# Kernel optimization log

Hardware: AMD Instinct MI355X
Metric: run time of the kernel (lower is better)

Reference implementation:

```python
import jax, jax.numpy as jnp
import numpy as np

# --- static config (lmax = mmax = 2, m-prime coefficient layout) ---
L = 2
NCOEF = (L + 1) ** 2            # 9 coeffs; m-prime order: m=0 -> l=0,1,2 | m=1 -> (-,+) x l=1,2 | m=2 -> (-,+) x l=2
GATE_IDX = jnp.array([0, 1, 0, 1, 0, 1, 1, 1])  # (l-1) of each non-scalar coeff in m-prime order
N_NODES = 10000
N_EDGES = 50000
C_SPH = 128
C_HID = 128
C_EDGE = 128
EXTRA_M0 = L * C_HID            # gate scalars emitted by conv1's m=0 branch


def _silu(x):
    return x * jax.nn.sigmoid(x)


def _layernorm(x, g, b, eps=1e-5):
    mu = jnp.mean(x, axis=-1, keepdims=True)
    var = jnp.var(x, axis=-1, keepdims=True)
    return (x - mu) * jax.lax.rsqrt(var + eps) * g + b


def _radial(x_edge, w1, b1, g, beta, w2, b2):
    # RadialFunction: Linear -> LayerNorm -> SiLU -> Linear, emits per-edge channel weights [E, 6*c_in]
    h = _silu(_layernorm(x_edge @ w1 + b1, g, beta))
    return h @ w2 + b2


def _so2_conv(feat, rad, w0, b0, w1, w2, c_in, c_out, extra):
    # feat: [E, 9, c_in] in m-prime order. Block-diagonal SO2 conv with per-edge radial modulation.
    E = feat.shape[0]
    # m = 0 block (3 real coeffs) -> dense linear, optionally emits extra gating scalars
    x0 = feat[:, 0:3].reshape(E, 3 * c_in) * rad[:, : 3 * c_in]
    y0 = x0 @ w0 + b0                                   # [E, 3*c_out + extra]
    out0 = y0[:, : 3 * c_out].reshape(E, 3, c_out)
    x_extra = y0[:, 3 * c_out:]
    # m = 1 block: coeffs 3:7 -> [E, 2(sign), 2(l)*c_in], complex-structured matmul
    x1 = feat[:, 3:7].reshape(E, 2, 2 * c_in) * rad[:, 3 * c_in: 5 * c_in][:, None, :]
    y1 = x1 @ w1                                        # [E, 2, 4*c_out]
    h = 2 * c_out
    r, i = y1[..., :h], y1[..., h:]
    out1 = jnp.stack([r[:, 0] - i[:, 1], r[:, 1] + i[:, 0]], axis=1).reshape(E, 4, c_out)
    # m = 2 block: coeffs 7:9 -> [E, 2(sign), 1(l)*c_in]
    x2 = feat[:, 7:9].reshape(E, 2, c_in) * rad[:, 5 * c_in: 6 * c_in][:, None, :]
    y2 = x2 @ w2                                        # [E, 2, 2*c_out]
    r, i = y2[..., :c_out], y2[..., c_out:]
    out2 = jnp.stack([r[:, 0] - i[:, 1], r[:, 1] + i[:, 0]], axis=1).reshape(E, 2, c_out)
    return jnp.concatenate([out0, out1, out2], axis=1), x_extra


def _gate(gating, feat):
    # GateActivation (m_prime=True): SiLU on l=0 scalar, SiLU(gates) broadcast per-degree on l>0 coeffs
    E = feat.shape[0]
    g = _silu(gating).reshape(E, L, C_HID)[:, GATE_IDX]  # [E, 8, C_HID]
    return jnp.concatenate([_silu(feat[:, :1]), feat[:, 1:] * g], axis=1)


def setup_inputs() -> dict:
    key = jax.random.key(0)
    ks = jax.random.split(key, 16)

    def nrm(k, shape, scale=1.0):
        return jax.random.normal(k, shape, dtype=jnp.float32) * scale

    C, H, CE = C_SPH, C_HID, C_EDGE
    return {
        "x": nrm(ks[0], (N_NODES, NCOEF, C)),
        "x_edge": nrm(ks[1], (N_EDGES, CE)),
        "edge_distance": jax.random.uniform(ks[2], (N_EDGES,), dtype=jnp.float32),
        "edge_index": jax.random.randint(ks[3], (2, N_EDGES), 0, N_NODES),
        "wigner": nrm(ks[4], (N_EDGES, NCOEF, NCOEF), 0.3),
        "wigner_inv": nrm(ks[5], (N_EDGES, NCOEF, NCOEF), 0.3),
        # radial MLP 1 (edge embed -> 6*C_SPH per-edge weights)
        "rad1_w1": nrm(ks[6], (CE, CE), CE ** -0.5),
        "rad1_b1": jnp.zeros((CE,), jnp.float32),
        "rad1_g": jnp.ones((CE,), jnp.float32),
        "rad1_beta": jnp.zeros((CE,), jnp.float32),
        "rad1_w2": nrm(ks[7], (CE, 6 * C), CE ** -0.5),
        "rad1_b2": jnp.zeros((6 * C,), jnp.float32),
        # SO2 conv 1 (sphere -> hidden, + gate scalars)
        "c1_w0": nrm(ks[8], (3 * C, 3 * H + EXTRA_M0), (3 * C) ** -0.5),
        "c1_b0": jnp.zeros((3 * H + EXTRA_M0,), jnp.float32),
        "c1_w1": nrm(ks[9], (2 * C, 4 * H), (2 * C) ** -0.5),
        "c1_w2": nrm(ks[10], (C, 2 * H), C ** -0.5),
        # radial MLP 2 (edge embed -> 6*C_HID per-edge weights)
        "rad2_w1": nrm(ks[11], (CE, CE), CE ** -0.5),
        "rad2_b1": jnp.zeros((CE,), jnp.float32),
        "rad2_g": jnp.ones((CE,), jnp.float32),
        "rad2_beta": jnp.zeros((CE,), jnp.float32),
        "rad2_w2": nrm(ks[12], (CE, 6 * H), CE ** -0.5),
        "rad2_b2": jnp.zeros((6 * H,), jnp.float32),
        # SO2 conv 2 (hidden -> sphere)
        "c2_w0": nrm(ks[13], (3 * H, 3 * C), (3 * H) ** -0.5),
        "c2_b0": jnp.zeros((3 * C,), jnp.float32),
        "c2_w1": nrm(ks[14], (2 * H, 4 * C), (2 * H) ** -0.5),
        "c2_w2": nrm(ks[15], (H, 2 * C), H ** -0.5),
    }


def reference(x, x_edge, edge_distance, edge_index, wigner, wigner_inv,
              rad1_w1, rad1_b1, rad1_g, rad1_beta, rad1_w2, rad1_b2,
              c1_w0, c1_b0, c1_w1, c1_w2,
              rad2_w1, rad2_b1, rad2_g, rad2_beta, rad2_w2, rad2_b2,
              c2_w0, c2_b0, c2_w1, c2_w2):
    src, dst = edge_index[0], edge_index[1]
    # gather source node features + per-edge Wigner rotation into m-prime layout: [E, 9, C_SPH]
    msg = jnp.einsum('erf,efc->erc', wigner, x[src])
    rad1 = _radial(x_edge, rad1_w1, rad1_b1, rad1_g, rad1_beta, rad1_w2, rad1_b2)
    msg, gating = _so2_conv(msg, rad1, c1_w0, c1_b0, c1_w1, c1_w2, C_SPH, C_HID, EXTRA_M0)
    msg = _gate(gating, msg)
    rad2 = _radial(x_edge, rad2_w1, rad2_b1, rad2_g, rad2_beta, rad2_w2, rad2_b2)
    msg, _ = _so2_conv(msg, rad2, c2_w0, c2_b0, c2_w1, c2_w2, C_HID, C_SPH, 0)
    # rotate back to the global frame and scatter-sum onto destination nodes
    msg = jnp.einsum('efr,erc->efc', wigner_inv, msg)
    return jax.ops.segment_sum(msg, dst, num_segments=x.shape[0])
```

## Files before the change

kernel.cpp:

```cpp
#include <hip/hip_runtime.h>
#include <hip/hip_bf16.h>

#define EDGES 50000
#define NODES 10000

typedef __hip_bfloat16 bf16;
typedef __attribute__((ext_vector_type(8))) short bf16x8v;
typedef __attribute__((ext_vector_type(4))) float f32x4;

__device__ __forceinline__ float bf2f(bf16 v){ return __bfloat162float(v); }
__device__ __forceinline__ bf16  f2bf(float v){ return __float2bfloat16(v); }
__device__ __forceinline__ unsigned short f2bfu(float f){
  bf16 h = __float2bfloat16(f);
  union{ bf16 h; unsigned short s; } u; u.h = h; return u.s;
}
__device__ __forceinline__ float silu_f(float v){ return v * (1.0f/(1.0f+__expf(-v))); }

__device__ __forceinline__ unsigned mul1(unsigned a, unsigned b){
  union{unsigned u; float f;} a0,a1,b0,b1;
  a0.u = (a & 0xffffu) << 16; a1.u = a & 0xffff0000u;
  b0.u = (b & 0xffffu) << 16; b1.u = b & 0xffff0000u;
  float p0 = a0.f*b0.f, p1 = a1.f*b1.f;
  return (unsigned)f2bfu(p0) | ((unsigned)f2bfu(p1) << 16);
}
__device__ __forceinline__ uint4 mulp(uint4 a, uint4 b){
  uint4 r; r.x=mul1(a.x,b.x); r.y=mul1(a.y,b.y); r.z=mul1(a.z,b.z); r.w=mul1(a.w,b.w); return r;
}

__global__ __launch_bounds__(256)
void k_wT(const float* __restrict__ w, bf16* __restrict__ wt, int K, int N){
  __shared__ float tile[32][33];
  const int kb = blockIdx.x*32, nb = blockIdx.y*32;
  const int tx = threadIdx.x & 31, ty = threadIdx.x >> 5;
#pragma unroll
  for (int i=0;i<32;i+=8) tile[ty+i][tx] = w[(size_t)(kb+ty+i)*N + nb+tx];
  __syncthreads();
#pragma unroll
  for (int i=0;i<32;i+=8) wt[(size_t)(nb+ty+i)*K + kb+tx] = f2bf(tile[tx][ty+i]);
}

__global__ __launch_bounds__(128)
void k_gather_rot(const float* __restrict__ x, const int* __restrict__ eidx,
                  const float* __restrict__ wig, bf16* __restrict__ msg)
{
  const int e = blockIdx.x;
  const int c = threadIdx.x;
  __shared__ float wl[81];
  if (c < 81) wl[c] = wig[e*81 + c];
  const int src = eidx[e];
  const float* xp = x + (size_t)src*1152 + c;
  float xr[9];
#pragma unroll
  for (int f=0; f<9; ++f) xr[f] = xp[f*128];
  __syncthreads();
  bf16* mp = msg + (size_t)e*1152 + c;
#pragma unroll
  for (int fo=0; fo<9; ++fo){
    float a = 0.f;
#pragma unroll
    for (int f=0; f<9; ++f) a = fmaf(wl[fo*9+f], xr[f], a);
    mp[fo*128] = f2bf(a);
  }
}

__global__ __launch_bounds__(256)
void k_radial(const float* __restrict__ x_edge,
              const float* __restrict__ w1, const float* __restrict__ b1,
              const float* __restrict__ gm, const float* __restrict__ bt,
              const float* __restrict__ w2, const float* __restrict__ b2,
              bf16* __restrict__ ro)
{
  __shared__ float xe[16][128];
  __shared__ float h[16][128];
  __shared__ float mu_s[16], rs_s[16];
  const int t = threadIdx.x;
  const int e0 = blockIdx.x * 16;
  for (int i=0;i<8;++i){
    int lin = t + 256*i;
    int e = lin >> 7, j2 = lin & 127;
    xe[e][j2] = x_edge[(size_t)(e0+e)*128 + j2];
  }
  __syncthreads();
  const int j = t & 127, g = t >> 7;
  {
    float acc[8] = {0,0,0,0,0,0,0,0};
    for (int k=0;k<128;k+=4){
      float wv0 = w1[(k+0)*128+j];
      float wv1 = w1[(k+1)*128+j];
      float wv2 = w1[(k+2)*128+j];
      float wv3 = w1[(k+3)*128+j];
#pragma unroll
      for (int e=0;e<8;++e){
        float4 xv = *(const float4*)&xe[g*8+e][k];
        acc[e] += xv.x*wv0 + xv.y*wv1 + xv.z*wv2 + xv.w*wv3;
      }
    }
    float bv = b1[j];
#pragma unroll
    for (int e=0;e<8;++e) h[g*8+e][j] = acc[e] + bv;
  }
  __syncthreads();
  {
    int e = t >> 4, p = t & 15;
    float s=0.f, ss=0.f;
#pragma unroll
    for (int i=0;i<8;++i){ float v = h[e][p+16*i]; s += v; ss += v*v; }
#pragma unroll
    for (int off=8; off>0; off>>=1){ s += __shfl_xor(s, off, 16); ss += __shfl_xor(ss, off, 16); }
    if (p==0){
      float m = s*(1.f/128.f);
      mu_s[e] = m;
      rs_s[e] = rsqrtf(fmaxf(ss*(1.f/128.f)-m*m, 0.f) + 1e-5f);
    }
  }
  __syncthreads();
  {
    float gv = gm[j], bv = bt[j];
#pragma unroll
    for (int e=0;e<8;++e){
      int ee = g*8+e;
      float v = (h[ee][j]-mu_s[ee])*rs_s[ee]*gv + bv;
      h[ee][j] = silu_f(v);
    }
  }
  __syncthreads();
  if (t < 192){
    int col = t*4;
    float acc[16][4];
#pragma unroll
    for (int e=0;e<16;++e){ acc[e][0]=acc[e][1]=acc[e][2]=acc[e][3]=0.f; }
    for (int k=0;k<128;k+=4){
      float4 wv0 = *(const float4*)&w2[(k+0)*768+col];
      float4 wv1 = *(const float4*)&w2[(k+1)*768+col];
      float4 wv2 = *(const float4*)&w2[(k+2)*768+col];
      float4 wv3 = *(const float4*)&w2[(k+3)*768+col];
#pragma unroll
      for (int e=0;e<16;++e){
        float4 hv = *(const float4*)&h[e][k];
        acc[e][0] += hv.x*wv0.x + hv.y*wv1.x + hv.z*wv2.x + hv.w*wv3.x;
        acc[e][1] += hv.x*wv0.y + hv.y*wv1.y + hv.z*wv2.y + hv.w*wv3.y;
        acc[e][2] += hv.x*wv0.z + hv.y*wv1.z + hv.z*wv2.z + hv.w*wv3.z;
        acc[e][3] += hv.x*wv0.w + hv.y*wv1.w + hv.z*wv2.w + hv.w*wv3.w;
      }
    }
    float4 bv = *(const float4*)&b2[col];
#pragma unroll
    for (int e=0;e<16;++e){
      ushort4 pk;
      pk.x = f2bfu(acc[e][0]+bv.x);
      pk.y = f2bfu(acc[e][1]+bv.y);
      pk.z = f2bfu(acc[e][2]+bv.z);
      pk.w = f2bfu(acc[e][3]+bv.w);
      *reinterpret_cast<ushort4*>(&ro[(size_t)(e0+e)*768 + col]) = pk;
    }
  }
}


template<bool CONV1>
__global__ __launch_bounds__(256, 3)
void k_g0(const bf16* __restrict__ rad, const bf16* __restrict__ msg_in,
          const bf16* __restrict__ w0t, const float* __restrict__ b0,
          bf16* __restrict__ msg, bf16* __restrict__ glb)
{
  __shared__ char ldsA[24576];
  __shared__ bf16 gls[8192];
  const int t = threadIdx.x;
  const int lane = t & 63, wv = t >> 6;
  const int lrow = lane & 15, lhi = lane >> 4;
  const int e0 = blockIdx.x * 32;
  int evalid = EDGES - e0; if (evalid > 32) evalid = 32;
  const uint4 z4 = {0u,0u,0u,0u};
  const f32x4 zf = {0.f,0.f,0.f,0.f};

#pragma unroll
  for (int i=0;i<6;++i){
    int ch = t + 256*i;
    int row = ch / 48, k0 = (ch % 48) * 8;
    int e = e0 + row;
    uint4 mz = z4, rz = z4;
    if (e < EDGES){
      mz = *(const uint4*)(msg_in + (size_t)e*1152 + k0);
      rz = *(const uint4*)(rad    + (size_t)e*768  + k0);
    }
    *(uint4*)(ldsA + ((row*768 + k0*2) ^ ((row&7)<<4))) = mulp(mz, rz);
  }
  __syncthreads();

  constexpr int NT0 = CONV1 ? 10 : 6;
  constexpr int HB  = NT0 / 2;
  const int wcol0 = wv * NT0 * 16;
  f32x4 acc0[NT0][2];
#pragma unroll
  for (int nt=0; nt<NT0; ++nt){ acc0[nt][0]=zf; acc0[nt][1]=zf; }
  for (int ks=0; ks<12; ++ks){
    bf16x8v a0 = *(const bf16x8v*)(ldsA + (((lrow   )*768 + ks*64 + lhi*16) ^ ((lrow&7)<<4)));
    bf16x8v a1 = *(const bf16x8v*)(ldsA + (((16+lrow)*768 + ks*64 + lhi*16) ^ ((lrow&7)<<4)));
#pragma unroll
    for (int h=0; h<2; ++h){
      bf16x8v bb[HB];
#pragma unroll
      for (int j=0;j<HB;++j){
        int coln = wcol0 + (h*HB+j)*16 + lrow;
        bb[j] = *(const bf16x8v*)(w0t + (size_t)coln*384 + ks*32 + lhi*8);
      }
#pragma unroll
      for (int j=0;j<HB;++j){
        int nt = h*HB+j;
        acc0[nt][0] = __builtin_amdgcn_mfma_f32_16x16x32_bf16(a0, bb[j], acc0[nt][0], 0,0,0);
        acc0[nt][1] = __builtin_amdgcn_mfma_f32_16x16x32_bf16(a1, bb[j], acc0[nt][1], 0,0,0);
      }
    }
  }
  if (CONV1){
#pragma unroll
    for (int nt=0; nt<NT0; ++nt){
      int colb = wcol0 + nt*16;
      if (colb >= 384){
        float bc = b0[colb + lrow];
        int cc = colb + lrow - 384;
#pragma unroll
        for (int mt=0; mt<2; ++mt)
#pragma unroll
        for (int r=0; r<4; ++r){
          int el = mt*16 + lhi*4 + r;
          bf16 gv = f2bf(silu_f(acc0[nt][mt][r] + bc));
          gls[el*256 + cc] = gv;
          if (el < evalid) glb[(size_t)(e0+el)*256 + cc] = gv;
        }
      }
    }
    __syncthreads();
  }
#pragma unroll
  for (int nt=0; nt<NT0; ++nt){
    int colb = wcol0 + nt*16;
    if (colb < 384){
      int col = colb + lrow;
      int f = col >> 7, c = col & 127;
      float bc = b0[col];
#pragma unroll
      for (int mt=0; mt<2; ++mt)
#pragma unroll
      for (int r=0; r<4; ++r){
        int el = mt*16 + lhi*4 + r;
        if (el < evalid){
          float v = acc0[nt][mt][r] + bc;
          float o;
          if (CONV1) o = (f==0) ? silu_f(v) : v * bf2f(gls[el*256 + (f==2?128:0) + c]);
          else       o = v;
          msg[(size_t)(e0+el)*1152 + col] = f2bf(o);
        }
      }
    }
  }
}

template<bool CONV1>
__global__ __launch_bounds__(256, 3)
void k_g1(const bf16* __restrict__ rad,
          const bf16* __restrict__ w1t,
          bf16* __restrict__ msg, const bf16* __restrict__ glb)
{
  __shared__ char ldsA[16384];
  const int t = threadIdx.x;
  const int lane = t & 63, wv = t >> 6;
  const int lrow = lane & 15, lhi = lane >> 4;
  const int e0 = blockIdx.x * 16;
  const uint4 z4 = {0u,0u,0u,0u};
  const f32x4 zf = {0.f,0.f,0.f,0.f};

#pragma unroll
  for (int i=0;i<4;++i){
    int ch = t + 256*i;
    int row = ch >> 5, k0 = (ch & 31) * 8;
    int e = e0 + (row >> 1);
    uint4 mz = z4, rz = z4;
    if (e < EDGES){
      mz = *(const uint4*)(msg + (size_t)e*1152 + 384 + (row&1)*256 + k0);
      rz = *(const uint4*)(rad + (size_t)e*768  + 384 + k0);
    }
    *(uint4*)(ldsA + ((row*512 + k0*2) ^ ((row&7)<<4))) = mulp(mz, rz);
  }
  __syncthreads();

  f32x4 acc1[4][2][2];
#pragma unroll
  for (int p=0;p<4;++p){ acc1[p][0][0]=zf; acc1[p][0][1]=zf; acc1[p][1][0]=zf; acc1[p][1][1]=zf; }
  for (int ks=0; ks<8; ++ks){
    bf16x8v aA[2];
#pragma unroll
    for (int m2=0; m2<2; ++m2){
      int row = m2*16 + lrow;
      aA[m2] = *(const bf16x8v*)(ldsA + ((row*512 + ks*64 + lhi*16) ^ ((row&7)<<4)));
    }
    bf16x8v br[4], bi[4];
#pragma unroll
    for (int p=0; p<4; ++p){
      int jj = wv*64 + p*16 + lrow;
      br[p] = *(const bf16x8v*)(w1t + (size_t)jj*256       + ks*32 + lhi*8);
      bi[p] = *(const bf16x8v*)(w1t + (size_t)(jj+256)*256 + ks*32 + lhi*8);
    }
#pragma unroll
    for (int p=0; p<4; ++p)
#pragma unroll
    for (int m2=0;m2<2;++m2){
      acc1[p][m2][0] = __builtin_amdgcn_mfma_f32_16x16x32_bf16(aA[m2], br[p], acc1[p][m2][0], 0,0,0);
      acc1[p][m2][1] = __builtin_amdgcn_mfma_f32_16x16x32_bf16(aA[m2], bi[p], acc1[p][m2][1], 0,0,0);
    }
  }
#pragma unroll
  for (int p=0;p<4;++p)
#pragma unroll
  for (int m2=0;m2<2;++m2)
#pragma unroll
  for (int re=0;re<2;++re){
    int elL = m2*8 + lhi*2 + re;
    int e = e0 + elL;
    if (e < EDGES){
      float r0 = acc1[p][m2][0][2*re+0], r1 = acc1[p][m2][0][2*re+1];
      float i0 = acc1[p][m2][1][2*re+0], i1 = acc1[p][m2][1][2*re+1];
      float o0 = r0 - i1, o1 = r1 + i0;
      int jj = wv*64 + p*16 + lrow;
      if (CONV1){ float g = bf2f(glb[(size_t)e*256 + jj]); o0 *= g; o1 *= g; }
      size_t base = (size_t)e*1152;
      msg[base + 384 + jj] = f2bf(o0);
      msg[base + 640 + jj] = f2bf(o1);
    }
  }
}

template<bool CONV1>
__global__ __launch_bounds__(256, 3)
void k_g2(const bf16* __restrict__ rad,
          const bf16* __restrict__ w2t,
          bf16* __restrict__ msg, const bf16* __restrict__ glb)
{
  __shared__ char ldsA[16384];
  const int t = threadIdx.x;
  const int lane = t & 63, wv = t >> 6;
  const int lrow = lane & 15, lhi = lane >> 4;
  const int e0 = blockIdx.x * 32;
  const uint4 z4 = {0u,0u,0u,0u};
  const f32x4 zf = {0.f,0.f,0.f,0.f};

#pragma unroll
  for (int i=0;i<4;++i){
    int ch = t + 256*i;
    int row = ch >> 4, k0 = (ch & 15) * 8;
    int e = e0 + (row >> 1);
    uint4 mz = z4, rz = z4;
    if (e < EDGES){
      mz = *(const uint4*)(msg + (size_t)e*1152 + 896 + (row&1)*128 + k0);
      rz = *(const uint4*)(rad + (size_t)e*768  + 640 + k0);
    }
    *(uint4*)(ldsA + ((row*256 + k0*2) ^ ((row&7)<<4))) = mulp(mz, rz);
  }
  __syncthreads();

  f32x4 acc2[2][4][2];
#pragma unroll
  for (int p=0;p<2;++p)
#pragma unroll
  for (int mt=0;mt<4;++mt){ acc2[p][mt][0]=zf; acc2[p][mt][1]=zf; }
  for (int ks=0; ks<4; ++ks){
    bf16x8v aA[4];
#pragma unroll
    for (int mt=0;mt<4;++mt){
      int row = mt*16 + lrow;
      aA[mt] = *(const bf16x8v*)(ldsA + ((row*256 + ks*64 + lhi*16) ^ ((row&7)<<4)));
    }
    bf16x8v br2[2], bi2[2];
#pragma unroll
    for (int p=0;p<2;++p){
      int jj = wv*32 + p*16 + lrow;
      br2[p] = *(const bf16x8v*)(w2t + (size_t)jj*128       + ks*32 + lhi*8);
      bi2[p] = *(const bf16x8v*)(w2t + (size_t)(jj+128)*128 + ks*32 + lhi*8);
    }
#pragma unroll
    for (int p=0;p<2;++p)
#pragma unroll
    for (int mt=0;mt<4;++mt){
      acc2[p][mt][0] = __builtin_amdgcn_mfma_f32_16x16x32_bf16(aA[mt], br2[p], acc2[p][mt][0], 0,0,0);
      acc2[p][mt][1] = __builtin_amdgcn_mfma_f32_16x16x32_bf16(aA[mt], bi2[p], acc2[p][mt][1], 0,0,0);
    }
  }
#pragma unroll
  for (int p=0;p<2;++p)
#pragma unroll
  for (int mt=0;mt<4;++mt)
#pragma unroll
  for (int re=0;re<2;++re){
    int el = mt*8 + lhi*2 + re;
    int e = e0 + el;
    if (e < EDGES){
      float r0 = acc2[p][mt][0][2*re+0], r1 = acc2[p][mt][0][2*re+1];
      float i0 = acc2[p][mt][1][2*re+0], i1 = acc2[p][mt][1][2*re+1];
      float o0 = r0 - i1, o1 = r1 + i0;
      int jj = wv*32 + p*16 + lrow;
      if (CONV1){ float g = bf2f(glb[(size_t)e*256 + 128 + jj]); o0 *= g; o1 *= g; }
      size_t base = (size_t)e*1152;
      msg[base + 896  + jj] = f2bf(o0);
      msg[base + 1024 + jj] = f2bf(o1);
    }
  }
}

__global__ __launch_bounds__(128)
void k_wiginv_scatter(const bf16* __restrict__ msg, const int* __restrict__ eidx,
                      const float* __restrict__ wiginv, float* __restrict__ out)
{
  const int e = blockIdx.x;
  const int c = threadIdx.x;
  __shared__ float wl[81];
  if (c < 81) wl[c] = wiginv[e*81 + c];
  float m[9];
#pragma unroll
  for (int r=0;r<9;++r) m[r] = bf2f(msg[(size_t)e*1152 + r*128 + c]);
  const int dst = eidx[EDGES + e];
  __syncthreads();
  float* op = out + (size_t)dst*1152 + c;
#pragma unroll
  for (int f=0;f<9;++f){
    float a = 0.f;
#pragma unroll
    for (int r=0;r<9;++r) a = fmaf(wl[f*9+r], m[r], a);
    atomicAdd(op + f*128, a);
  }
}

extern "C" void kernel_launch(void* const* d_in, const int* in_sizes, int n_in,
                              void* d_out, int out_size, void* d_ws, size_t ws_size,
                              hipStream_t stream)
{
  const float* x       = (const float*)d_in[0];
  const float* x_edge  = (const float*)d_in[1];
  const int*   eidx    = (const int*)  d_in[3];
  const float* wig     = (const float*)d_in[4];
  const float* wiginv  = (const float*)d_in[5];
  const float* r1w1    = (const float*)d_in[6];
  const float* r1b1    = (const float*)d_in[7];
  const float* r1g     = (const float*)d_in[8];
  const float* r1bt    = (const float*)d_in[9];
  const float* r1w2    = (const float*)d_in[10];
  const float* r1b2    = (const float*)d_in[11];
  const float* c1w0    = (const float*)d_in[12];
  const float* c1b0    = (const float*)d_in[13];
  const float* c1w1    = (const float*)d_in[14];
  const float* c1w2    = (const float*)d_in[15];
  const float* r2w1    = (const float*)d_in[16];
  const float* r2b1    = (const float*)d_in[17];
  const float* r2g     = (const float*)d_in[18];
  const float* r2bt    = (const float*)d_in[19];
  const float* r2w2    = (const float*)d_in[20];
  const float* r2b2    = (const float*)d_in[21];
  const float* c2w0    = (const float*)d_in[22];
  const float* c2b0    = (const float*)d_in[23];
  const float* c2w1    = (const float*)d_in[24];
  const float* c2w2    = (const float*)d_in[25];
  float* out = (float*)d_out;

  char* ws = (char*)d_ws;
  bf16* msg  = (bf16*)(ws);
  bf16* rad  = (bf16*)(ws + (size_t)115200000);
  bf16* w0t1 = (bf16*)(ws + (size_t)192000000);
  bf16* w1t1 = (bf16*)(ws + (size_t)192491520);
  bf16* w2t1 = (bf16*)(ws + (size_t)192753664);
  bf16* w0t2 = (bf16*)(ws + (size_t)192819200);
  bf16* w1t2 = (bf16*)(ws + (size_t)193114112);
  bf16* w2t2 = (bf16*)(ws + (size_t)193376256);
  bf16* glb  = (bf16*)(ws + (size_t)193441792);

  k_wT<<<dim3(12,20),256,0,stream>>>(c1w0, w0t1, 384, 640);
  k_wT<<<dim3( 8,16),256,0,stream>>>(c1w1, w1t1, 256, 512);
  k_wT<<<dim3( 4, 8),256,0,stream>>>(c1w2, w2t1, 128, 256);
  k_wT<<<dim3(12,12),256,0,stream>>>(c2w0, w0t2, 384, 384);
  k_wT<<<dim3( 8,16),256,0,stream>>>(c2w1, w1t2, 256, 512);
  k_wT<<<dim3( 4, 8),256,0,stream>>>(c2w2, w2t2, 128, 256);

  hipMemsetAsync(d_out, 0, (size_t)out_size*sizeof(float), stream);
  k_gather_rot<<<EDGES, 128, 0, stream>>>(x, eidx, wig, msg);

  k_radial<<<EDGES/16, 256, 0, stream>>>(x_edge, r1w1, r1b1, r1g, r1bt, r1w2, r1b2, rad);
  k_g0<true ><<<(EDGES+31)/32, 256, 0, stream>>>(rad, msg, w0t1, c1b0, msg, glb);
  k_g1<true ><<<(EDGES+15)/16, 256, 0, stream>>>(rad, w1t1, msg, glb);
  k_g2<true ><<<(EDGES+31)/32, 256, 0, stream>>>(rad, w2t1, msg, glb);

  k_radial<<<EDGES/16, 256, 0, stream>>>(x_edge, r2w1, r2b1, r2g, r2bt, r2w2, r2b2, rad);
  k_g0<false><<<(EDGES+31)/32, 256, 0, stream>>>(rad, msg, w0t2, c2b0, msg, glb);
  k_g1<false><<<(EDGES+15)/16, 256, 0, stream>>>(rad, w1t2, msg, glb);
  k_g2<false><<<(EDGES+31)/32, 256, 0, stream>>>(rad, w2t2, msg, glb);

  k_wiginv_scatter<<<EDGES, 128, 0, stream>>>(msg, eidx, wiginv, out);
}
```

Baseline: 1.416 ms.

## Rewrite radial MLP kernel to use bf16 MFMA with transposed weights

```diff
diff --git a/kernel.cpp b/kernel.cpp
--- a/kernel.cpp
+++ b/kernel.cpp
@@ -13,6 +13,9 @@
 __device__ __forceinline__ unsigned short f2bfu(float f){
   bf16 h = __float2bfloat16(f);
   union{ bf16 h; unsigned short s; } u; u.h = h; return u.s;
+}
+__device__ __forceinline__ unsigned packbf2(float a, float b){
+  return (unsigned)f2bfu(a) | ((unsigned)f2bfu(b) << 16);
 }
 __device__ __forceinline__ float silu_f(float v){ return v * (1.0f/(1.0f+__expf(-v))); }
 
@@ -63,95 +66,132 @@
   }
 }
 
-__global__ __launch_bounds__(256)
-void k_radial(const float* __restrict__ x_edge,
-              const float* __restrict__ w1, const float* __restrict__ b1,
-              const float* __restrict__ gm, const float* __restrict__ bt,
-              const float* __restrict__ w2, const float* __restrict__ b2,
-              bf16* __restrict__ ro)
-{
-  __shared__ float xe[16][128];
-  __shared__ float h[16][128];
-  __shared__ float mu_s[16], rs_s[16];
+__global__ __launch_bounds__(256, 3)
+void k_radial_mfma(const float* __restrict__ x_edge,
+                   const bf16* __restrict__ w1t, const float* __restrict__ b1,
+                   const float* __restrict__ gm, const float* __restrict__ bt,
+                   const bf16* __restrict__ w2t, const float* __restrict__ b2,
+                   bf16* __restrict__ ro)
+{
+  __shared__ char ldsA[16384];
+  __shared__ float lb1[128], lg[128], lbt[128];
   const int t = threadIdx.x;
-  const int e0 = blockIdx.x * 16;
-  for (int i=0;i<8;++i){
-    int lin = t + 256*i;
-    int e = lin >> 7, j2 = lin & 127;
-    xe[e][j2] = x_edge[(size_t)(e0+e)*128 + j2];
-  }
-  __syncthreads();
-  const int j = t & 127, g = t >> 7;
-  {
-    float acc[8] = {0,0,0,0,0,0,0,0};
-    for (int k=0;k<128;k+=4){
-      float wv0 = w1[(k+0)*128+j];
-      float wv1 = w1[(k+1)*128+j];
-      float wv2 = w1[(k+2)*128+j];
-      float wv3 = w1[(k+3)*128+j];
-#pragma unroll
-      for (int e=0;e<8;++e){
-        float4 xv = *(const float4*)&xe[g*8+e][k];
-        acc[e] += xv.x*wv0 + xv.y*wv1 + xv.z*wv2 + xv.w*wv3;
-      }
-    }
-    float bv = b1[j];
-#pragma unroll
-    for (int e=0;e<8;++e) h[g*8+e][j] = acc[e] + bv;
-  }
-  __syncthreads();
-  {
-    int e = t >> 4, p = t & 15;
-    float s=0.f, ss=0.f;
-#pragma unroll
-    for (int i=0;i<8;++i){ float v = h[e][p+16*i]; s += v; ss += v*v; }
-#pragma unroll
-    for (int off=8; off>0; off>>=1){ s += __shfl_xor(s, off, 16); ss += __shfl_xor(ss, off, 16); }
-    if (p==0){
-      float m = s*(1.f/128.f);
-      mu_s[e] = m;
-      rs_s[e] = rsqrtf(fmaxf(ss*(1.f/128.f)-m*m, 0.f) + 1e-5f);
-    }
-  }
-  __syncthreads();
-  {
-    float gv = gm[j], bv = bt[j];
-#pragma unroll
-    for (int e=0;e<8;++e){
-      int ee = g*8+e;
-      float v = (h[ee][j]-mu_s[ee])*rs_s[ee]*gv + bv;
-      h[ee][j] = silu_f(v);
-    }
-  }
-  __syncthreads();
-  if (t < 192){
-    int col = t*4;
-    float acc[16][4];
-#pragma unroll
-    for (int e=0;e<16;++e){ acc[e][0]=acc[e][1]=acc[e][2]=acc[e][3]=0.f; }
-    for (int k=0;k<128;k+=4){
-      float4 wv0 = *(const float4*)&w2[(k+0)*768+col];
-      float4 wv1 = *(const float4*)&w2[(k+1)*768+col];
-      float4 wv2 = *(const float4*)&w2[(k+2)*768+col];
-      float4 wv3 = *(const float4*)&w2[(k+3)*768+col];
-#pragma unroll
-      for (int e=0;e<16;++e){
-        float4 hv = *(const float4*)&h[e][k];
-        acc[e][0] += hv.x*wv0.x + hv.y*wv1.x + hv.z*wv2.x + hv.w*wv3.x;
-        acc[e][1] += hv.x*wv0.y + hv.y*wv1.y + hv.z*wv2.y + hv.w*wv3.y;
-        acc[e][2] += hv.x*wv0.z + hv.y*wv1.z + hv.z*wv2.z + hv.w*wv3.z;
-        acc[e][3] += hv.x*wv0.w + hv.y*wv1.w + hv.z*wv2.w + hv.w*wv3.w;
-      }
-    }
-    float4 bv = *(const float4*)&b2[col];
-#pragma unroll
-    for (int e=0;e<16;++e){
-      ushort4 pk;
-      pk.x = f2bfu(acc[e][0]+bv.x);
-      pk.y = f2bfu(acc[e][1]+bv.y);
-      pk.z = f2bfu(acc[e][2]+bv.z);
-      pk.w = f2bfu(acc[e][3]+bv.w);
-      *reinterpret_cast<ushort4*>(&ro[(size_t)(e0+e)*768 + col]) = pk;
+  const int lane = t & 63, wv = t >> 6;
+  const int lrow = lane & 15, lhi = lane >> 4;
+  const int e0 = blockIdx.x * 64;
+  int evalid = EDGES - e0; if (evalid > 64) evalid = 64;
+  const f32x4 zf = {0.f,0.f,0.f,0.f};
+
+  if (t < 128){ lb1[t] = b1[t]; lg[t] = gm[t]; lbt[t] = bt[t]; }
+#pragma unroll
+  for (int i=0;i<2;++i){
+    int ch = t + 256*i;
+    int row = ch >> 3, k0 = (ch & 7) * 16;
+    int e = e0 + row;
+    uint4 o = {0u,0u,0u,0u};
+    uint4 o2 = {0u,0u,0u,0u};
+    if (e < EDGES){
+      const float* xp = x_edge + (size_t)e*128 + k0;
+      float4 a0 = *(const float4*)(xp+0), a1 = *(const float4*)(xp+4);
+      float4 a2 = *(const float4*)(xp+8), a3 = *(const float4*)(xp+12);
+      o.x  = packbf2(a0.x,a0.y); o.y  = packbf2(a0.z,a0.w);
+      o.z  = packbf2(a1.x,a1.y); o.w  = packbf2(a1.z,a1.w);
+      o2.x = packbf2(a2.x,a2.y); o2.y = packbf2(a2.z,a2.w);
+      o2.z = packbf2(a3.x,a3.y); o2.w = packbf2(a3.z,a3.w);
+    }
+    *(uint4*)(ldsA + ((row*256 + k0*2     ) ^ ((row&7)<<4))) = o;
+    *(uint4*)(ldsA + ((row*256 + k0*2 + 16) ^ ((row&7)<<4))) = o2;
+  }
+  __syncthreads();
+
+  f32x4 acc[8];
+#pragma unroll
+  for (int nt=0;nt<8;++nt) acc[nt] = zf;
+  for (int ks=0; ks<4; ++ks){
+    int row = wv*16 + lrow;
+    bf16x8v a0 = *(const bf16x8v*)(ldsA + ((row*256 + ks*64 + lhi*16) ^ ((row&7)<<4)));
+    bf16x8v bb[4];
+#pragma unroll
+    for (int h=0; h<2; ++h){
+#pragma unroll
+      for (int j=0;j<4;++j){
+        int jj = (h*4+j)*16 + lrow;
+        bb[j] = *(const bf16x8v*)(w1t + (size_t)jj*128 + ks*32 + lhi*8);
+      }
+#pragma unroll
+      for (int j=0;j<4;++j)
+        acc[h*4+j] = __builtin_amdgcn_mfma_f32_16x16x32_bf16(a0, bb[j], acc[h*4+j], 0,0,0);
+    }
+  }
+#pragma unroll
+  for (int nt=0;nt<8;++nt){
+    float bv = lb1[nt*16 + lrow];
+#pragma unroll
+    for (int r=0;r<4;++r) acc[nt][r] += bv;
+  }
+  float mu[4], rs[4];
+#pragma unroll
+  for (int r=0;r<4;++r){
+    float s = 0.f, ss = 0.f;
+#pragma unroll
+    for (int nt=0;nt<8;++nt){ float v = acc[nt][r]; s += v; ss += v*v; }
+#pragma unroll
+    for (int off=1; off<16; off<<=1){ s += __shfl_xor(s, off, 16); ss += __shfl_xor(ss, off, 16); }
+    float m = s*(1.f/128.f);
+    mu[r] = m;
+    rs[r] = rsqrtf(fmaxf(ss*(1.f/128.f) - m*m, 0.f) + 1e-5f);
+  }
+#pragma unroll
+  for (int nt=0;nt<8;++nt){
+    int col = nt*16 + lrow;
+    float gv = lg[col], bv = lbt[col];
+#pragma unroll
+    for (int r=0;r<4;++r){
+      int row = wv*16 + lhi*4 + r;
+      float v = (acc[nt][r] - mu[r]) * rs[r] * gv + bv;
+      *(bf16*)(ldsA + ((row*256 + col*2) ^ ((row&7)<<4))) = f2bf(silu_f(v));
+    }
+  }
+  __syncthreads();
+
+#pragma unroll
+  for (int c=0;c<3;++c){
+    f32x4 a2[4][4];
+#pragma unroll
+    for (int p=0;p<4;++p)
+#pragma unroll
+    for (int mt=0;mt<4;++mt) a2[p][mt] = zf;
+    for (int ks=0; ks<4; ++ks){
+      bf16x8v aA[4];
+#pragma unroll
+      for (int mt=0;mt<4;++mt){
+        int row = mt*16 + lrow;
+        aA[mt] = *(const bf16x8v*)(ldsA + ((row*256 + ks*64 + lhi*16) ^ ((row&7)<<4)));
+      }
+      bf16x8v bb[4];
+#pragma unroll
+      for (int p=0;p<4;++p){
+        int jj = wv*192 + c*64 + p*16 + lrow;
+        bb[p] = *(const bf16x8v*)(w2t + (size_t)jj*128 + ks*32 + lhi*8);
+      }
+#pragma unroll
+      for (int p=0;p<4;++p)
+#pragma unroll
+      for (int mt=0;mt<4;++mt)
+        a2[p][mt] = __builtin_amdgcn_mfma_f32_16x16x32_bf16(aA[mt], bb[p], a2[p][mt], 0,0,0);
+    }
+#pragma unroll
+    for (int p=0;p<4;++p){
+      int col = wv*192 + c*64 + p*16 + lrow;
+      float bc = b2[col];
+#pragma unroll
+      for (int mt=0;mt<4;++mt)
+#pragma unroll
+      for (int r=0;r<4;++r){
+        int el = mt*16 + lhi*4 + r;
+        if (el < evalid)
+          ro[(size_t)(e0+el)*768 + col] = f2bf(a2[p][mt][r] + bc);
+      }
     }
   }
 }
@@ -461,15 +501,19 @@
   float* out = (float*)d_out;
 
   char* ws = (char*)d_ws;
-  bf16* msg  = (bf16*)(ws);
-  bf16* rad  = (bf16*)(ws + (size_t)115200000);
-  bf16* w0t1 = (bf16*)(ws + (size_t)192000000);
-  bf16* w1t1 = (bf16*)(ws + (size_t)192491520);
-  bf16* w2t1 = (bf16*)(ws + (size_t)192753664);
-  bf16* w0t2 = (bf16*)(ws + (size_t)192819200);
-  bf16* w1t2 = (bf16*)(ws + (size_t)193114112);
-  bf16* w2t2 = (bf16*)(ws + (size_t)193376256);
-  bf16* glb  = (bf16*)(ws + (size_t)193441792);
+  bf16* msg   = (bf16*)(ws);
+  bf16* rad   = (bf16*)(ws + (size_t)115200000);
+  bf16* w0t1  = (bf16*)(ws + (size_t)192000000);
+  bf16* w1t1  = (bf16*)(ws + (size_t)192491520);
+  bf16* w2t1  = (bf16*)(ws + (size_t)192753664);
+  bf16* w0t2  = (bf16*)(ws + (size_t)192819200);
+  bf16* w1t2  = (bf16*)(ws + (size_t)193114112);
+  bf16* w2t2  = (bf16*)(ws + (size_t)193376256);
+  bf16* rw1tA = (bf16*)(ws + (size_t)193441792);
+  bf16* rw2tA = (bf16*)(ws + (size_t)193474560);
+  bf16* rw1tB = (bf16*)(ws + (size_t)193671168);
+  bf16* rw2tB = (bf16*)(ws + (size_t)193703936);
+  bf16* glb   = (bf16*)(ws + (size_t)193900544);
 
   k_wT<<<dim3(12,20),256,0,stream>>>(c1w0, w0t1, 384, 640);
   k_wT<<<dim3( 8,16),256,0,stream>>>(c1w1, w1t1, 256, 512);
@@ -477,16 +521,20 @@
   k_wT<<<dim3(12,12),256,0,stream>>>(c2w0, w0t2, 384, 384);
   k_wT<<<dim3( 8,16),256,0,stream>>>(c2w1, w1t2, 256, 512);
   k_wT<<<dim3( 4, 8),256,0,stream>>>(c2w2, w2t2, 128, 256);
+  k_wT<<<dim3( 4, 4),256,0,stream>>>(r1w1, rw1tA, 128, 128);
+  k_wT<<<dim3( 4,24),256,0,stream>>>(r1w2, rw2tA, 128, 768);
+  k_wT<<<dim3( 4, 4),256,0,stream>>>(r2w1, rw1tB, 128, 128);
+  k_wT<<<dim3( 4,24),256,0,stream>>>(r2w2, rw2tB, 128, 768);
 
   hipMemsetAsync(d_out, 0, (size_t)out_size*sizeof(float), stream);
   k_gather_rot<<<EDGES, 128, 0, stream>>>(x, eidx, wig, msg);
 
-  k_radial<<<EDGES/16, 256, 0, stream>>>(x_edge, r1w1, r1b1, r1g, r1bt, r1w2, r1b2, rad);
+  k_radial_mfma<<<(EDGES+63)/64, 256, 0, stream>>>(x_edge, rw1tA, r1b1, r1g, r1bt, rw2tA, r1b2, rad);
   k_g0<true ><<<(EDGES+31)/32, 256, 0, stream>>>(rad, msg, w0t1, c1b0, msg, glb);
   k_g1<true ><<<(EDGES+15)/16, 256, 0, stream>>>(rad, w1t1, msg, glb);
   k_g2<true ><<<(EDGES+31)/32, 256, 0, stream>>>(rad, w2t1, msg, glb);
 
-  k_radial<<<EDGES/16, 256, 0, stream>>>(x_edge, r2w1, r2b1, r2g, r2bt, r2w2, r2b2, rad);
+  k_radial_mfma<<<(EDGES+63)/64, 256, 0, stream>>>(x_edge, rw1tB, r2b1, r2g, r2bt, rw2tB, r2b2, rad);
   k_g0<false><<<(EDGES+31)/32, 256, 0, stream>>>(rad, msg, w0t2, c2b0, msg, glb);
   k_g1<false><<<(EDGES+15)/16, 256, 0, stream>>>(rad, w1t2, msg, glb);
   k_g2<false><<<(EDGES+31)/32, 256, 0, stream>>>(rad, w2t2, msg, glb);
```

After: 1.222 ms. 13.7% less time.
